# Optimization experiments

Hardware: AMD Instinct MI355X
Metric: run time of the kernel (lower is better)

The kernel has to match this reference:

```python
import jax, jax.numpy as jnp
import numpy as np

N_NODES = 100_000
N_EDGES = 1_600_000
NFEAT = 16          # nfeature_dim
HID = 128           # hidden_dim
K = 3               # TAGConv hops in pretrained convs
N_LAYERS = 4        # pretrained n_gnn_layers (1 in->hid + 3 hid->hid)
OUT_DIM = 1


def _gcn_norm(edge_index, n):
    # PyG TAGConv: symmetric gcn_norm WITHOUT self-loops (k=0 term covers self).
    row, col = edge_index[0], edge_index[1]
    deg = jax.ops.segment_sum(jnp.ones((edge_index.shape[1],), jnp.float32), col, num_segments=n)
    dis = jnp.where(deg > 0, jax.lax.rsqrt(jnp.maximum(deg, 1.0)), 0.0)
    return dis[row] * dis[col]


def _tagconv(x, row, col, norm, ws, b, n):
    # out = sum_k (A_hat^k x) W_k + b ; ws: [K+1, in, out]
    out = x @ ws[0]
    h = x
    for k in range(1, ws.shape[0]):
        h = jax.ops.segment_sum(h[row] * norm[:, None], col, num_segments=n)
        out = out + h @ ws[k]
    return out + b


def setup_inputs() -> dict:
    key = jax.random.key(0)
    ks = jax.random.split(key, 10)
    x = jax.random.normal(ks[0], (N_NODES, NFEAT + 1), jnp.float32)
    edge_index = jax.random.randint(ks[1], (2, N_EDGES), 0, N_NODES, dtype=jnp.int64)
    # featureEmbedding: TAGConv(17 -> 16, K=1) -> 2 weight mats + bias
    fe_ws = jax.random.normal(ks[2], (2, NFEAT + 1, NFEAT), jnp.float32) * (NFEAT + 1) ** -0.5
    fe_b = jnp.zeros((NFEAT,), jnp.float32)
    # convs[0]: TAGConv(16 -> 128, K=3)
    conv0_ws = jax.random.normal(ks[3], (K + 1, NFEAT, HID), jnp.float32) * NFEAT ** -0.5
    conv0_b = jnp.zeros((HID,), jnp.float32)
    # convs[1..3]: TAGConv(128 -> 128, K=3), stacked
    conv_ws = jax.random.normal(ks[4], (N_LAYERS - 1, K + 1, HID, HID), jnp.float32) * HID ** -0.5
    conv_b = jnp.zeros((N_LAYERS - 1, HID), jnp.float32)
    fc_w = jax.random.normal(ks[5], (HID, OUT_DIM), jnp.float32) * HID ** -0.5
    fc_b = jnp.zeros((OUT_DIM,), jnp.float32)
    return {"x": x, "edge_index": edge_index, "fe_ws": fe_ws, "fe_b": fe_b,
            "conv0_ws": conv0_ws, "conv0_b": conv0_b,
            "conv_ws": conv_ws, "conv_b": conv_b, "fc_w": fc_w, "fc_b": fc_b}


def reference(x, edge_index, fe_ws, fe_b, conv0_ws, conv0_b, conv_ws, conv_b, fc_w, fc_b):
    n = x.shape[0]
    row, col = edge_index[0], edge_index[1]
    norm = _gcn_norm(edge_index, n)
    # featureEmbedding (K=1)
    h = _tagconv(x, row, col, norm, fe_ws, fe_b, n)
    # convs[0..n-2] with dropout (eval-mode identity) + ReLU
    h = _tagconv(h, row, col, norm, conv0_ws, conv0_b, n)
    h = jax.nn.relu(h)
    for i in range(conv_ws.shape[0] - 1):
        h = _tagconv(h, row, col, norm, conv_ws[i], conv_b[i], n)
        h = jax.nn.relu(h)
    # last conv: no dropout/relu
    h = _tagconv(h, row, col, norm, conv_ws[-1], conv_b[-1], n)
    return h @ fc_w + fc_b
```

## Files before the change

### kernel.cpp

```cpp
#include <hip/hip_runtime.h>

#define NN 100000
#define NE 1600000
#define SCAN_B 98
#define NB 782
#define SUBCAP 512
#define MAXB 4096

typedef _Float16 half8 __attribute__((ext_vector_type(8)));
typedef float f32x4 __attribute__((ext_vector_type(4)));
struct h2s { _Float16 x, y; };
struct h4s { _Float16 a, b, c, d; };

__global__ void k_deg(const int* __restrict__ col, int* __restrict__ degi) {
  int e = blockIdx.x * blockDim.x + threadIdx.x;
  if (e < NE) atomicAdd(&degi[col[e]], 1);
}

__global__ void k_dis(const int* __restrict__ degi, float* __restrict__ dis) {
  int i = blockIdx.x * blockDim.x + threadIdx.x;
  if (i < NN) {
    int d = degi[i];
    dis[i] = d > 0 ? rsqrtf((float)d) : 0.0f;
  }
}

__global__ void k_scan1(const int* __restrict__ degi, int* __restrict__ bsum) {
  __shared__ int red[256];
  int t = threadIdx.x;
  int base = blockIdx.x * 1024 + t * 4;
  int s = 0;
#pragma unroll
  for (int u = 0; u < 4; ++u) {
    int i = base + u;
    if (i < NN) s += degi[i];
  }
  red[t] = s;
  __syncthreads();
  for (int o = 128; o; o >>= 1) {
    if (t < o) red[t] += red[t + o];
    __syncthreads();
  }
  if (t == 0) bsum[blockIdx.x] = red[0];
}

__global__ void k_scan2(const int* __restrict__ bsum, int* __restrict__ boff,
                        int* __restrict__ off) {
  __shared__ int sh[128];
  int t = threadIdx.x;
  int v = (t < SCAN_B) ? bsum[t] : 0;
  sh[t] = v;
  __syncthreads();
  for (int o = 1; o < 128; o <<= 1) {
    int u = (t >= o) ? sh[t - o] : 0;
    __syncthreads();
    sh[t] += u;
    __syncthreads();
  }
  if (t < SCAN_B) boff[t] = sh[t] - v;
  if (t == 127) off[NN] = sh[127];
}

__global__ void k_scan3(const int* __restrict__ degi, const int* __restrict__ boff,
                        int* __restrict__ off) {
  __shared__ int red[256];
  int t = threadIdx.x;
  int base = blockIdx.x * 1024 + t * 4;
  int d[4];
  int s = 0;
#pragma unroll
  for (int u = 0; u < 4; ++u) {
    int i = base + u;
    d[u] = (i < NN) ? degi[i] : 0;
    s += d[u];
  }
  red[t] = s;
  __syncthreads();
  for (int o = 1; o < 256; o <<= 1) {
    int u2 = (t >= o) ? red[t - o] : 0;
    __syncthreads();
    red[t] += u2;
    __syncthreads();
  }
  int pre = red[t] - s + boff[blockIdx.x];
#pragma unroll
  for (int u = 0; u < 4; ++u) {
    int i = base + u;
    if (i < NN) {
      off[i] = pre;
      pre += d[u];
    }
  }
}

__global__ void k_bscatter(const int* __restrict__ row, const int* __restrict__ col,
                           int* __restrict__ bcur, unsigned* __restrict__ pk2) {
  int e = blockIdx.x * blockDim.x + threadIdx.x;
  int x = blockIdx.x & 7;
  if (e < NE) {
    int c = col[e];
    int cell = ((c >> 7) << 3) | x;
    int slot = atomicAdd(&bcur[cell * 16], 1);
    slot = min(slot, SUBCAP - 1);
    pk2[(size_t)cell * SUBCAP + slot] = (unsigned)row[e] | ((unsigned)(c & 127) << 17);
  }
}

__global__ __launch_bounds__(256) void k_bsort(const unsigned* __restrict__ pk2,
                                               const int* __restrict__ bcur,
                                               const int* __restrict__ off,
                                               const float* __restrict__ dis,
                                               int* __restrict__ src,
                                               _Float16* __restrict__ wh) {
  __shared__ unsigned epk[MAXB];
  __shared__ int cnt[128];
  __shared__ int sc[128];
  __shared__ int cur[128];
  __shared__ float sdis[128];
  __shared__ int soff[9];
  int b = blockIdx.x;
  int n0 = b << 7;
  int gb = off[n0];
  int t = threadIdx.x;
  if (t == 0) {
    int acc = 0;
#pragma unroll
    for (int x = 0; x < 8; ++x) {
      soff[x] = acc;
      acc += min(bcur[((b << 3) | x) * 16], SUBCAP);
    }
    soff[8] = acc;
  }
  if (t < 128) {
    cnt[t] = 0;
    sdis[t] = (n0 + t < NN) ? dis[n0 + t] : 0.f;
  }
  __syncthreads();
  int m = soff[8];
#pragma unroll
  for (int x = 0; x < 8; ++x) {
    int c0 = soff[x], c1 = soff[x + 1];
    const unsigned* seg = &pk2[(size_t)((b << 3) | x) * SUBCAP];
    for (int i = c0 + t; i < c1; i += 256) epk[i] = seg[i - c0];
  }
  __syncthreads();
  for (int i = t; i < m; i += 256) atomicAdd(&cnt[epk[i] >> 17], 1);
  __syncthreads();
  if (t < 128) sc[t] = cnt[t];
  __syncthreads();
  for (int o = 1; o < 128; o <<= 1) {
    int u = (t < 128 && t >= o) ? sc[t - o] : 0;
    __syncthreads();
    if (t < 128) sc[t] += u;
    __syncthreads();
  }
  if (t < 128) cur[t] = sc[t] - cnt[t];
  __syncthreads();
  for (int i = t; i < m; i += 256) {
    unsigned p = epk[i];
    int c = (int)(p >> 17);
    int r = (int)(p & 0x1FFFFu);
    int pos = gb + atomicAdd(&cur[c], 1);
    src[pos] = r;
    wh[pos] = (_Float16)(dis[r] * sdis[c]);
  }
}

__global__ void k_wprep(const float* __restrict__ cw, _Float16* __restrict__ wt) {
  int i = blockIdx.x * 256 + threadIdx.x;
  if (i < 12 * 16384) {
    int mat = i >> 14;
    int rem = i & 16383;
    int k = rem >> 7;
    int n = rem & 127;
    wt[(mat << 14) | (n << 7) | k] = (_Float16)cw[i];
  }
}

__global__ void k_uprep(const float* __restrict__ cw, const float* __restrict__ cb,
                        const float* __restrict__ fcw, const float* __restrict__ fcb,
                        float* __restrict__ uvec, float* __restrict__ cval) {
  int i = blockIdx.x * 256 + threadIdx.x;
  if (i < 512) {
    int s = i >> 7, k = i & 127;
    const float* W = cw + (size_t)(8 + s) * 16384 + k * 128;
    float acc = 0.f;
    for (int n = 0; n < 128; ++n) acc += W[n] * fcw[n];
    uvec[i] = acc;
  }
  if (i == 512) {
    float acc = 0.f;
    for (int n = 0; n < 128; ++n) acc += cb[2 * 128 + n] * fcw[n];
    *cval = acc + fcb[0];
  }
}

__global__ void k_prop16h(const h2s* __restrict__ h, const int* __restrict__ off,
                          const int* __restrict__ src, const _Float16* __restrict__ wh,
                          h2s* __restrict__ out) {
  int t = threadIdx.x;
  int node = blockIdx.x * 8 + (t >> 3);
  int f = t & 7;
  int b = off[node], e = off[node + 1];
  float ax = 0.f, ay = 0.f;
  int j = b;
  for (; j + 2 <= e; j += 2) {
    int s0 = src[j], s1 = src[j + 1];
    float w0 = (float)wh[j], w1 = (float)wh[j + 1];
    h2s v0 = h[s0 * 8 + f];
    h2s v1 = h[s1 * 8 + f];
    ax = fmaf((float)v0.x, w0, fmaf((float)v1.x, w1, ax));
    ay = fmaf((float)v0.y, w0, fmaf((float)v1.y, w1, ay));
  }
  if (j < e) {
    int s = src[j];
    float w = (float)wh[j];
    h2s v = h[s * 8 + f];
    ax = fmaf((float)v.x, w, ax);
    ay = fmaf((float)v.y, w, ay);
  }
  h2s o;
  o.x = (_Float16)ax;
  o.y = (_Float16)ay;
  unsigned bits;
  __builtin_memcpy(&bits, &o, 4);
  __builtin_nontemporal_store(bits, (unsigned*)&out[node * 8 + f]);
}

__global__ __launch_bounds__(128) void k_prop128h(const h2s* __restrict__ h,
                                                  const int* __restrict__ off,
                                                  const int* __restrict__ src,
                                                  const _Float16* __restrict__ wh,
                                                  h2s* __restrict__ out) {
  int wid = __builtin_amdgcn_readfirstlane(threadIdx.x >> 6);
  int node = blockIdx.x * 2 + wid;
  int t = threadIdx.x & 63;
  int b = off[node], e = off[node + 1];
  float ax = 0.f, ay = 0.f;
  int j = b;
  for (; j + 8 <= e; j += 8) {
    h2s v[8];
    float w[8];
#pragma unroll
    for (int u = 0; u < 8; ++u) {
      v[u] = h[src[j + u] * 64 + t];
      w[u] = (float)wh[j + u];
    }
#pragma unroll
    for (int u = 0; u < 8; ++u) {
      ax = fmaf((float)v[u].x, w[u], ax);
      ay = fmaf((float)v[u].y, w[u], ay);
    }
  }
  for (; j < e; ++j) {
    int s = src[j];
    float w = (float)wh[j];
    h2s v = h[s * 64 + t];
    ax = fmaf((float)v.x, w, ax);
    ay = fmaf((float)v.y, w, ay);
  }
  h2s o;
  o.x = (_Float16)ax;
  o.y = (_Float16)ay;
  unsigned bits;
  __builtin_memcpy(&bits, &o, 4);
  __builtin_nontemporal_store(bits, (unsigned*)&out[node * 64 + t]);
}

template <bool RELU>
__global__ __launch_bounds__(256) void k_tag4_mfma(
    const _Float16* __restrict__ A0, const _Float16* __restrict__ A1,
    const _Float16* __restrict__ A2, const _Float16* __restrict__ A3,
    const _Float16* __restrict__ Wt, const float* __restrict__ bias,
    _Float16* __restrict__ out) {
  __shared__ _Float16 Wl[16384];
  int tid = threadIdx.x;
  int wid = tid >> 6;
  int lane = tid & 63;
  int r = lane & 15, kg = lane >> 4;
  int m0 = blockIdx.x * 128 + wid * 32;
  int row0 = min(m0 + r, NN - 1);
  int row1 = min(m0 + 16 + r, NN - 1);
  f32x4 acc0[8] = {}, acc1[8] = {};
  const _Float16* As[4] = {A0, A1, A2, A3};
#pragma unroll
  for (int s = 0; s < 4; ++s) {
    const float4* Wg = (const float4*)(Wt + (s << 14));
    __syncthreads();
#pragma unroll
    for (int u = 0; u < 8; ++u) {
      int g = tid + u * 256;
      int sg = g ^ ((g >> 4) & 7);
      *(float4*)((char*)Wl + g * 16) = Wg[sg];
    }
    __syncthreads();
    const _Float16* A = As[s];
    half8 a0[4], a1[4];
#pragma unroll
    for (int kc = 0; kc < 4; ++kc) {
      int kbase = kc * 32 + kg * 8;
      a0[kc] = *(const half8*)&A[(size_t)row0 * 128 + kbase];
      a1[kc] = *(const half8*)&A[(size_t)row1 * 128 + kbase];
    }
#pragma unroll
    for (int kc = 0; kc < 4; ++kc) {
      int kb2 = (kc * 32 + kg * 8) * 2;
#pragma unroll
      for (int nb = 0; nb < 8; ++nb) {
        int n = nb * 16 + r;
        int ba = ((n << 8) + kb2) ^ ((n & 7) << 4);
        half8 b = *(const half8*)((const char*)Wl + ba);
        acc0[nb] = __builtin_amdgcn_mfma_f32_16x16x32_f16(a0[kc], b, acc0[nb], 0, 0, 0);
        acc1[nb] = __builtin_amdgcn_mfma_f32_16x16x32_f16(a1[kc], b, acc1[nb], 0, 0, 0);
      }
    }
  }
  int ccol = lane & 15;
#pragma unroll
  for (int h = 0; h < 2; ++h) {
    int crow0 = m0 + h * 16 + kg * 4;
#pragma unroll
    for (int nb = 0; nb < 8; ++nb) {
      int col = nb * 16 + ccol;
      float bv = bias[col];
      const f32x4& av = h ? acc1[nb] : acc0[nb];
#pragma unroll
      for (int e = 0; e < 4; ++e) {
        float v = av[e] + bv;
        if (RELU) v = fmaxf(v, 0.f);
        int rr = crow0 + e;
        if (rr < NN) out[(size_t)rr * 128 + col] = (_Float16)v;
      }
    }
  }
}

__global__ void k_tagfc(const _Float16* __restrict__ A0, const _Float16* __restrict__ A1,
                        const _Float16* __restrict__ A2, const _Float16* __restrict__ A3,
                        const float* __restrict__ uvec, const float* __restrict__ cval,
                        float* __restrict__ out) {
  int node = blockIdx.x;
  int t = threadIdx.x;
  const h2s* As[4] = {(const h2s*)A0, (const h2s*)A1, (const h2s*)A2, (const h2s*)A3};
  float s = 0.f;
#pragma unroll
  for (int q = 0; q < 4; ++q) {
    h2s v = As[q][(size_t)node * 64 + t];
    float2 u = ((const float2*)(uvec + (q << 7)))[t];
    s = fmaf((float)v.x, u.x, fmaf((float)v.y, u.y, s));
  }
  for (int o = 32; o; o >>= 1) s += __shfl_down(s, o);
  if (t == 0) out[node] = s + *cval;
}

__global__ __launch_bounds__(256) void k_conv0_fused(
    const _Float16* __restrict__ A0, const _Float16* __restrict__ A1,
    const _Float16* __restrict__ A2, const _Float16* __restrict__ A3,
    const float* __restrict__ W , const float* __restrict__ bias,
    _Float16* __restrict__ out) {
  __shared__ float Wl[4 * 16 * 128];
  for (int i = threadIdx.x * 4; i < 4 * 16 * 128; i += 1024)
    *(float4*)&Wl[i] = *(const float4*)&W[i];
  __syncthreads();
  int r0 = blockIdx.x * 32 + (threadIdx.x >> 5) * 4;
  int c0 = (threadIdx.x & 31) * 4;
  float acc[4][4] = {};
  const _Float16* As[4] = {A0, A1, A2, A3};
#pragma unroll
  for (int s = 0; s < 4; ++s) {
    const _Float16* A = As[s];
    const float* Ws = &Wl[s * 2048];
#pragma unroll
    for (int k = 0; k < 16; k += 4) {
      float4 w0 = *(const float4*)&Ws[(k + 0) * 128 + c0];
      float4 w1 = *(const float4*)&Ws[(k + 1) * 128 + c0];
      float4 w2 = *(const float4*)&Ws[(k + 2) * 128 + c0];
      float4 w3 = *(const float4*)&Ws[(k + 3) * 128 + c0];
#pragma unroll
      for (int i = 0; i < 4; ++i) {
        h4s a4 = *(const h4s*)&A[(r0 + i) * 16 + k];
        float ax = (float)a4.a, ay = (float)a4.b, az = (float)a4.c, aw = (float)a4.d;
        acc[i][0] = fmaf(ax, w0.x, fmaf(ay, w1.x, fmaf(az, w2.x, fmaf(aw, w3.x, acc[i][0]))));
        acc[i][1] = fmaf(ax, w0.y, fmaf(ay, w1.y, fmaf(az, w2.y, fmaf(aw, w3.y, acc[i][1]))));
        acc[i][2] = fmaf(ax, w0.z, fmaf(ay, w1.z, fmaf(az, w2.z, fmaf(aw, w3.z, acc[i][2]))));
        acc[i][3] = fmaf(ax, w0.w, fmaf(ay, w1.w, fmaf(az, w2.w, fmaf(aw, w3.w, acc[i][3]))));
      }
    }
  }
#pragma unroll
  for (int i = 0; i < 4; ++i) {
    h4s o;
    o.a = (_Float16)fmaxf(acc[i][0] + bias[c0 + 0], 0.f);
    o.b = (_Float16)fmaxf(acc[i][1] + bias[c0 + 1], 0.f);
    o.c = (_Float16)fmaxf(acc[i][2] + bias[c0 + 2], 0.f);
    o.d = (_Float16)fmaxf(acc[i][3] + bias[c0 + 3], 0.f);
    *(h4s*)&out[(size_t)(r0 + i) * 128 + c0] = o;
  }
}

template <int IN, bool ACCUM, bool BIAS>
__global__ void k_mm16h(const float* __restrict__ A, const float* __restrict__ W,
                        const float* __restrict__ bias, _Float16* __restrict__ C) {
  __shared__ float Wl[IN * 16];
  for (int i = threadIdx.x; i < IN * 16; i += 256) Wl[i] = W[i];
  __syncthreads();
  int r = blockIdx.x * 16 + (threadIdx.x >> 4);
  int c = threadIdx.x & 15;
  float acc = 0.f;
  for (int k = 0; k < IN; ++k) acc += A[r * IN + k] * Wl[k * 16 + c];
  int idx = r * 16 + c;
  if (BIAS) acc += bias[c];
  if (ACCUM) acc += (float)C[idx];
  C[idx] = (_Float16)acc;
}

extern "C" void kernel_launch(void* const* d_in, const int* in_sizes, int n_in,
                              void* d_out, int out_size, void* d_ws, size_t ws_size,
                              hipStream_t stream) {
  const float* x = (const float*)d_in[0];
  const int* ei = (const int*)d_in[1];
  const float* fe_ws = (const float*)d_in[2];
  const float* fe_b = (const float*)d_in[3];
  const float* c0_ws = (const float*)d_in[4];
  const float* c0_b = (const float*)d_in[5];
  const float* cw = (const float*)d_in[6];
  const float* cb = (const float*)d_in[7];
  const float* fcw = (const float*)d_in[8];
  const float* fcb = (const float*)d_in[9];
  float* out = (float*)d_out;

  const int* row = ei;
  const int* colv = ei + NE;

  char* wp = (char*)d_ws;
  auto alloc = [&](size_t bytes) {
    char* p = wp;
    wp += (bytes + 511) & ~(size_t)511;
    return p;
  };
  int* degi = (int*)alloc(NN * 4);
  int* off = (int*)alloc((NN + 1) * 4);
  int* bsum = (int*)alloc(SCAN_B * 4);
  int* boff = (int*)alloc(SCAN_B * 4);
  int* bcur = (int*)alloc((size_t)NB * 8 * 16 * 4);
  float* dis = (float*)alloc(NN * 4);
  int* src = (int*)alloc((size_t)NE * 4);
  unsigned* pk2 = (unsigned*)alloc((size_t)NB * 8 * SUBCAP * 4);
  _Float16* wh = (_Float16*)alloc((size_t)NE * 2);
  _Float16* wsT = (_Float16*)alloc((size_t)12 * 16384 * 2);
  float* uvec = (float*)alloc(512 * 4);
  float* cval = (float*)alloc(4);
  _Float16* y1h = (_Float16*)alloc((size_t)NN * 16 * 2);
  _Float16* h16 = (_Float16*)alloc((size_t)NN * 16 * 2);
  _Float16* p16b = (_Float16*)alloc((size_t)NN * 16 * 2);
  _Float16* p16c = (_Float16*)alloc((size_t)NN * 16 * 2);
  _Float16* p16d = (_Float16*)alloc((size_t)NN * 16 * 2);
  _Float16* H0 = (_Float16*)alloc((size_t)NN * 128 * 2);
  _Float16* H1 = (_Float16*)alloc((size_t)NN * 128 * 2);
  _Float16* T1 = (_Float16*)alloc((size_t)NN * 128 * 2);
  _Float16* T2 = (_Float16*)alloc((size_t)NN * 128 * 2);
  _Float16* T3 = (_Float16*)alloc((size_t)NN * 128 * 2);

  hipMemsetAsync(degi, 0, NN * 4, stream);
  hipMemsetAsync(bcur, 0, (size_t)NB * 8 * 16 * 4, stream);
  k_deg<<<(NE + 255) / 256, 256, 0, stream>>>(colv, degi);
  k_dis<<<(NN + 255) / 256, 256, 0, stream>>>(degi, dis);
  k_scan1<<<SCAN_B, 256, 0, stream>>>(degi, bsum);
  k_scan2<<<1, 128, 0, stream>>>(bsum, boff, off);
  k_scan3<<<SCAN_B, 256, 0, stream>>>(degi, boff, off);
  k_bscatter<<<(NE + 255) / 256, 256, 0, stream>>>(row, colv, bcur, pk2);
  k_bsort<<<NB, 256, 0, stream>>>(pk2, bcur, off, dis, src, wh);
  k_wprep<<<768, 256, 0, stream>>>(cw, wsT);
  k_uprep<<<3, 256, 0, stream>>>(cw, cb, fcw, fcb, uvec, cval);

  k_mm16h<17, false, false><<<NN / 16, 256, 0, stream>>>(x, fe_ws + 17 * 16, nullptr, y1h);
  k_prop16h<<<NN / 8, 64, 0, stream>>>((const h2s*)y1h, off, src, wh, (h2s*)h16);
  k_mm16h<17, true, true><<<NN / 16, 256, 0, stream>>>(x, fe_ws, fe_b, h16);

  k_prop16h<<<NN / 8, 64, 0, stream>>>((const h2s*)h16, off, src, wh, (h2s*)p16b);
  k_prop16h<<<NN / 8, 64, 0, stream>>>((const h2s*)p16b, off, src, wh, (h2s*)p16c);
  k_prop16h<<<NN / 8, 64, 0, stream>>>((const h2s*)p16c, off, src, wh, (h2s*)p16d);
  k_conv0_fused<<<NN / 32, 256, 0, stream>>>(h16, p16b, p16c, p16d, c0_ws, c0_b, H0);

  _Float16* hin = H0;
  _Float16* hout = H1;
  int mgrid = (NN + 127) / 128;
  int pgrid = NN / 2;
  for (int l = 0; l < 2; ++l) {
    k_prop128h<<<pgrid, 128, 0, stream>>>((const h2s*)hin, off, src, wh, (h2s*)T1);
    k_prop128h<<<pgrid, 128, 0, stream>>>((const h2s*)T1, off, src, wh, (h2s*)T2);
    k_prop128h<<<pgrid, 128, 0, stream>>>((const h2s*)T2, off, src, wh, (h2s*)T3);
    const _Float16* Wl = wsT + (size_t)l * 4 * 16384;
    const float* bl = cb + l * 128;
    k_tag4_mfma<true><<<mgrid, 256, 0, stream>>>(hin, T1, T2, T3, Wl, bl, hout);
    _Float16* t = hin; hin = hout; hout = t;
  }

  k_prop128h<<<pgrid, 128, 0, stream>>>((const h2s*)hin, off, src, wh, (h2s*)T1);
  k_prop128h<<<pgrid, 128, 0, stream>>>((const h2s*)T1, off, src, wh, (h2s*)T2);
  k_prop128h<<<pgrid, 128, 0, stream>>>((const h2s*)T2, off, src, wh, (h2s*)T3);
  k_tagfc<<<NN, 64, 0, stream>>>(hin, T1, T2, T3, uvec, cval, out);
}
```

Before: 945.3 us.

## Project last layer to scalars before propagation to avoid 128-wide hops

The last TAGConv layer is linear and followed by the fc layer, so the input is first projected onto the four combined weight vectors (uvec per hop). Only four scalars per node are then propagated through the graph instead of 128-wide half features. This replaces three 128-channel propagation passes with three tiny 4-channel passes plus a final combine. It relies on A^k commuting with the right-multiplication, and changes rounding order (fp32 scalars instead of fp16 features).

```diff
diff --git a/kernel.cpp b/kernel.cpp
--- a/kernel.cpp
+++ b/kernel.cpp
@@ -265,6 +265,51 @@
   unsigned bits;
   __builtin_memcpy(&bits, &o, 4);
   __builtin_nontemporal_store(bits, (unsigned*)&out[node * 64 + t]);
+}
+
+__global__ void k_dotz(const _Float16* __restrict__ h, const float* __restrict__ uvec,
+                       float4* __restrict__ Q) {
+  int node = blockIdx.x;
+  int t = threadIdx.x;
+  h2s v = ((const h2s*)h)[(size_t)node * 64 + t];
+  float p[4];
+#pragma unroll
+  for (int s = 0; s < 4; ++s) {
+    float2 u = ((const float2*)(uvec + (s << 7)))[t];
+    p[s] = fmaf((float)v.x, u.x, (float)v.y * u.y);
+  }
+#pragma unroll
+  for (int s = 0; s < 4; ++s)
+    for (int o = 32; o; o >>= 1) p[s] += __shfl_down(p[s], o);
+  if (t == 0) Q[node] = make_float4(p[0], p[1], p[2], p[3]);
+}
+
+__global__ __launch_bounds__(256) void k_zprop(const float* __restrict__ Qin,
+                                               const int* __restrict__ off,
+                                               const int* __restrict__ src,
+                                               const _Float16* __restrict__ wh,
+                                               float* __restrict__ Qout) {
+  int t = threadIdx.x;
+  int node = blockIdx.x * 64 + (t >> 2);
+  int comp = t & 3;
+  if (node >= NN) return;
+  int b = off[node], e = off[node + 1];
+  float acc = 0.f;
+  int j = b;
+  for (; j + 2 <= e; j += 2) {
+    int s0 = src[j], s1 = src[j + 1];
+    float w0 = (float)wh[j], w1 = (float)wh[j + 1];
+    acc = fmaf(Qin[s0 * 4 + comp], w0, fmaf(Qin[s1 * 4 + comp], w1, acc));
+  }
+  if (j < e) acc = fmaf(Qin[src[j] * 4 + comp], (float)wh[j], acc);
+  __builtin_nontemporal_store(acc, &Qout[node * 4 + comp]);
+}
+
+__global__ void k_zfinal(const float4* __restrict__ Q0, const float4* __restrict__ Q1,
+                         const float4* __restrict__ Q2, const float4* __restrict__ Q3,
+                         const float* __restrict__ cval, float* __restrict__ out) {
+  int n = blockIdx.x * 256 + threadIdx.x;
+  if (n < NN) out[n] = Q0[n].x + Q1[n].y + Q2[n].z + Q3[n].w + *cval;
 }
 
 template <bool RELU>
@@ -333,24 +378,6 @@
       }
     }
   }
-}
-
-__global__ void k_tagfc(const _Float16* __restrict__ A0, const _Float16* __restrict__ A1,
-                        const _Float16* __restrict__ A2, const _Float16* __restrict__ A3,
-                        const float* __restrict__ uvec, const float* __restrict__ cval,
-                        float* __restrict__ out) {
-  int node = blockIdx.x;
-  int t = threadIdx.x;
-  const h2s* As[4] = {(const h2s*)A0, (const h2s*)A1, (const h2s*)A2, (const h2s*)A3};
-  float s = 0.f;
-#pragma unroll
-  for (int q = 0; q < 4; ++q) {
-    h2s v = As[q][(size_t)node * 64 + t];
-    float2 u = ((const float2*)(uvec + (q << 7)))[t];
-    s = fmaf((float)v.x, u.x, fmaf((float)v.y, u.y, s));
-  }
-  for (int o = 32; o; o >>= 1) s += __shfl_down(s, o);
-  if (t == 0) out[node] = s + *cval;
 }
 
 __global__ __launch_bounds__(256) void k_conv0_fused(
@@ -450,6 +477,10 @@
   _Float16* wsT = (_Float16*)alloc((size_t)12 * 16384 * 2);
   float* uvec = (float*)alloc(512 * 4);
   float* cval = (float*)alloc(4);
+  float4* Q0 = (float4*)alloc((size_t)NN * 16);
+  float4* Q1 = (float4*)alloc((size_t)NN * 16);
+  float4* Q2 = (float4*)alloc((size_t)NN * 16);
+  float4* Q3 = (float4*)alloc((size_t)NN * 16);
   _Float16* y1h = (_Float16*)alloc((size_t)NN * 16 * 2);
   _Float16* h16 = (_Float16*)alloc((size_t)NN * 16 * 2);
   _Float16* p16b = (_Float16*)alloc((size_t)NN * 16 * 2);
@@ -496,8 +527,9 @@
     _Float16* t = hin; hin = hout; hout = t;
   }
 
-  k_prop128h<<<pgrid, 128, 0, stream>>>((const h2s*)hin, off, src, wh, (h2s*)T1);
-  k_prop128h<<<pgrid, 128, 0, stream>>>((const h2s*)T1, off, src, wh, (h2s*)T2);
-  k_prop128h<<<pgrid, 128, 0, stream>>>((const h2s*)T2, off, src, wh, (h2s*)T3);
-  k_tagfc<<<NN, 64, 0, stream>>>(hin, T1, T2, T3, uvec, cval, out);
-}
+  k_dotz<<<NN, 64, 0, stream>>>(hin, uvec, Q0);
+  k_zprop<<<(NN + 63) / 64, 256, 0, stream>>>((const float*)Q0, off, src, wh, (float*)Q1);
+  k_zprop<<<(NN + 63) / 64, 256, 0, stream>>>((const float*)Q1, off, src, wh, (float*)Q2);
+  k_zprop<<<(NN + 63) / 64, 256, 0, stream>>>((const float*)Q2, off, src, wh, (float*)Q3);
+  k_zfinal<<<(NN + 255) / 256, 256, 0, stream>>>(Q0, Q1, Q2, Q3, cval, out);
+}
```

After: 819.1 us. 13.4% less time.
